# Kernel optimization log

Measured on AMD Instinct MI355X. Metric: run time of the kernel, lower is better.

## Reference

```python
import jax, jax.numpy as jnp
import numpy as np

H = 256
EDGE_DIM = 16
B, N = 8, 4096
E = 524288
EPS = 1e-5


def setup_inputs() -> dict:
    key = jax.random.key(0)
    ks = jax.random.split(key, 16)
    s = 0.02
    return {
        "h": jax.random.normal(ks[0], (B, N, H), dtype=jnp.float32),
        "edge_index": jax.random.randint(ks[1], (2, E), 0, B * N, dtype=jnp.int64),
        "edge_attr": jax.random.normal(ks[2], (E, EDGE_DIM), dtype=jnp.float32),
        "mask": jnp.ones((B, N), dtype=jnp.float32),
        # message_net params
        "W1": jax.random.normal(ks[3], (2 * H + EDGE_DIM, H), dtype=jnp.float32) * s,
        "b1": jnp.zeros((H,), dtype=jnp.float32),
        "W2": jax.random.normal(ks[4], (H, H), dtype=jnp.float32) * s,
        "b2": jnp.zeros((H,), dtype=jnp.float32),
        # update_net params
        "U1": jax.random.normal(ks[5], (2 * H, H), dtype=jnp.float32) * s,
        "c1": jnp.zeros((H,), dtype=jnp.float32),
        "U2": jax.random.normal(ks[6], (H, H), dtype=jnp.float32) * s,
        "c2": jnp.zeros((H,), dtype=jnp.float32),
        # LayerNorm params
        "gamma": jnp.ones((H,), dtype=jnp.float32),
        "beta": jnp.zeros((H,), dtype=jnp.float32),
    }


def reference(h, edge_index, edge_attr, mask, W1, b1, W2, b2, U1, c1, U2, c2, gamma, beta):
    batch, n_nodes, hid = h.shape
    h_flat = h.reshape(-1, hid)                       # (B*N, H)
    src, dst = edge_index[0], edge_index[1]
    # gather -> message MLP
    msg_in = jnp.concatenate([h_flat[src], h_flat[dst], edge_attr], axis=-1)  # (E, 2H+16)
    messages = jax.nn.silu(msg_in @ W1 + b1) @ W2 + b2                        # (E, H)
    # scatter-add aggregation by destination node
    aggr = jax.ops.segment_sum(messages, dst, num_segments=batch * n_nodes)   # (B*N, H)
    # update MLP + residual (dropout = identity in eval mode)
    upd_in = jnp.concatenate([h_flat, aggr], axis=-1)                         # (B*N, 2H)
    h_new = h_flat + (jax.nn.silu(upd_in @ U1 + c1) @ U2 + c2)
    # LayerNorm over last dim
    mu = jnp.mean(h_new, axis=-1, keepdims=True)
    var = jnp.mean(jnp.square(h_new - mu), axis=-1, keepdims=True)
    h_new = (h_new - mu) * jax.lax.rsqrt(var + EPS) * gamma + beta
    return h_new.reshape(batch, n_nodes, hid) * mask[..., None]
```

## Files before the change

kernel.cpp:

```cpp
#include <hip/hip_runtime.h>

#define H_DIM 256
#define E_NUM 524288
#define NN    32768
#define K2    512
#define K2S   520
#define SAS   264
#define XS    264

typedef unsigned short u16;
typedef unsigned int   u32;
typedef __attribute__((ext_vector_type(8))) short s16x8;
typedef __attribute__((ext_vector_type(4))) float f32x4;
typedef __attribute__((ext_vector_type(4))) unsigned short u16x4;

__device__ __forceinline__ u16 f2b(float x) {
    u32 u = __float_as_uint(x);
    u32 r = (u + 0x7FFFu + ((u >> 16) & 1u)) >> 16;
    return (u16)r;
}
__device__ __forceinline__ float b2f(u16 v) {
    u32 u = ((u32)v) << 16;
    return __uint_as_float(u);
}
__device__ __forceinline__ void fma4(float4& acc, float s, const float4& vw) {
    acc.x += s * vw.x; acc.y += s * vw.y; acc.z += s * vw.z; acc.w += s * vw.w;
}

__global__ __launch_bounds__(256) void k_prep_w(
    const float* __restrict__ W1, const float* __restrict__ W2,
    const float* __restrict__ U1, const float* __restrict__ U2,
    u16* __restrict__ WpqT, u16* __restrict__ W2T,
    u16* __restrict__ U1T, u16* __restrict__ U2T) {
    int idx = blockIdx.x * 256 + threadIdx.x;
    if (idx < 131072) {
        int c = idx >> 8, k = idx & 255;
        float v = (c < 256) ? W1[k * 256 + c] : W1[(256 + k) * 256 + (c - 256)];
        WpqT[idx] = f2b(v);
    } else if (idx < 196608) {
        int i = idx - 131072; int c = i >> 8, k = i & 255;
        W2T[i] = f2b(W2[k * 256 + c]);
    } else if (idx < 327680) {
        int i = idx - 196608; int c = i >> 9, k = i & 511;
        U1T[i] = f2b(U1[(size_t)k * 256 + c]);
    } else if (idx < 393216) {
        int i = idx - 327680; int c = i >> 8, k = i & 255;
        U2T[i] = f2b(U2[k * 256 + c]);
    }
}

__global__ __launch_bounds__(256) void k_hist(const int* __restrict__ eidx,
                                              int* __restrict__ cnt) {
    int i = blockIdx.x * 256 + threadIdx.x;
    if (i < E_NUM) atomicAdd(&cnt[eidx[E_NUM + i]], 1);
}

__global__ __launch_bounds__(256) void k_scan(const int* __restrict__ cnt,
                                              int* __restrict__ base,
                                              int* __restrict__ nxt) {
    __shared__ int part[256];
    const int t = threadIdx.x;
    const int st = t * 128;
    int s = 0;
    for (int i = 0; i < 128; ++i) s += cnt[st + i];
    part[t] = s;
    __syncthreads();
    if (t == 0) {
        int r = 0;
        for (int i = 0; i < 256; ++i) { int v = part[i]; part[i] = r; r += v; }
        base[NN] = r;
    }
    __syncthreads();
    int off = part[t];
    for (int i = 0; i < 128; ++i) {
        int v = cnt[st + i];
        base[st + i] = off;
        nxt[st + i] = off;
        off += v;
    }
}

__global__ __launch_bounds__(256) void k_scatter(const int* __restrict__ eidx,
                                                 int* __restrict__ nxt,
                                                 int2* __restrict__ elist) {
    int i = blockIdx.x * 256 + threadIdx.x;
    if (i < E_NUM) {
        int d = eidx[E_NUM + i];
        int p = atomicAdd(&nxt[d], 1);
        elist[p] = make_int2(eidx[i], i);
    }
}

__global__ __launch_bounds__(256, 2) void k_gemm_pq(
    const float* __restrict__ h, const u16* __restrict__ WpqT,
    u16* __restrict__ PQ) {
    __shared__ __align__(16) u16 sA[64 * SAS];
    const int t = threadIdx.x;
    const int rowTile = blockIdx.x >> 1, q = blockIdx.x & 1;
    const int n0 = rowTile * 64;
    {
        const int r = t >> 2, g = t & 3;
        const float* hrow = h + (size_t)(n0 + r) * 256;
        u16* rowp = sA + r * SAS;
#pragma unroll
        for (int j = 0; j < 8; ++j) {
            const int c = g + 4 * j;
            float4 v0 = *reinterpret_cast<const float4*>(hrow + c * 8);
            float4 v1 = *reinterpret_cast<const float4*>(hrow + c * 8 + 4);
            s16x8 o;
            o[0] = (short)f2b(v0.x); o[1] = (short)f2b(v0.y);
            o[2] = (short)f2b(v0.z); o[3] = (short)f2b(v0.w);
            o[4] = (short)f2b(v1.x); o[5] = (short)f2b(v1.y);
            o[6] = (short)f2b(v1.z); o[7] = (short)f2b(v1.w);
            *reinterpret_cast<s16x8*>(rowp + c * 8) = o;
        }
    }
    __syncthreads();
    const int lane = t & 63, wv = t >> 6;
    const int l15 = lane & 15, l4 = lane >> 4;
    const int colBase = wv * 64 + l15;
    const f32x4 z4 = {0.f, 0.f, 0.f, 0.f};
    f32x4 acc[4][4];
#pragma unroll
    for (int m = 0; m < 4; ++m)
#pragma unroll
        for (int n = 0; n < 4; ++n) acc[m][n] = z4;
    {
        const u16* Bb = WpqT + (size_t)(q * 256 + colBase) * 256 + l4 * 8;
        for (int kk = 0; kk < 8; ++kk) {
            s16x8 a[4], b[4];
#pragma unroll
            for (int m = 0; m < 4; ++m)
                a[m] = *reinterpret_cast<const s16x8*>(sA + (m * 16 + l15) * SAS + kk * 32 + l4 * 8);
#pragma unroll
            for (int n = 0; n < 4; ++n)
                b[n] = *reinterpret_cast<const s16x8*>(Bb + (size_t)n * 16 * 256 + kk * 32);
#pragma unroll
            for (int m = 0; m < 4; ++m)
#pragma unroll
                for (int n = 0; n < 4; ++n)
                    acc[m][n] = __builtin_amdgcn_mfma_f32_16x16x32_bf16(a[m], b[n], acc[m][n], 0, 0, 0);
        }
    }
#pragma unroll
    for (int m = 0; m < 4; ++m)
#pragma unroll
        for (int j = 0; j < 4; ++j) {
            const int row = n0 + m * 16 + l4 * 4 + j;
            u16* op = PQ + (size_t)row * 512 + q * 256 + colBase;
#pragma unroll
            for (int n = 0; n < 4; ++n) op[n * 16] = f2b(acc[m][n][j]);
        }
}

__global__ __launch_bounds__(256, 4) void k_aggr(
    const u16* __restrict__ PQ, const int2* __restrict__ elist,
    const int* __restrict__ base, const float* __restrict__ ea,
    const float* __restrict__ W1, const float* __restrict__ b1,
    u16* __restrict__ Sb) {
    const int t = threadIdx.x, lane = t & 63, wv = t >> 6;
    const int d = blockIdx.x * 4 + wv;
    const int c0 = lane * 4;
    float4 Wr[16];
#pragma unroll
    for (int k = 0; k < 16; ++k)
        Wr[k] = *reinterpret_cast<const float4*>(W1 + (size_t)(512 + k) * 256 + c0);
    float4 qb = *reinterpret_cast<const float4*>(b1 + c0);
    {
        u16x4 qv = *reinterpret_cast<const u16x4*>(PQ + (size_t)d * 512 + 256 + c0);
        qb.x += b2f(qv.x); qb.y += b2f(qv.y); qb.z += b2f(qv.z); qb.w += b2f(qv.w);
    }
    const int e0 = base[d], e1 = base[d + 1];
    float4 acc = {0.f, 0.f, 0.f, 0.f};
    for (int cb = e0; cb < e1; cb += 64) {
        const int n = min(64, e1 - cb);
        int2 ee = make_int2(0, 0);
        if (lane < n) ee = elist[cb + lane];
        int src = __shfl(ee.x, 0), eid = __shfl(ee.y, 0);
        u16x4 pv = *reinterpret_cast<const u16x4*>(PQ + (size_t)src * 512 + c0);
        const float* ep = ea + (size_t)eid * 16;
        float4 a0 = *reinterpret_cast<const float4*>(ep);
        float4 a1 = *reinterpret_cast<const float4*>(ep + 4);
        float4 a2 = *reinterpret_cast<const float4*>(ep + 8);
        float4 a3 = *reinterpret_cast<const float4*>(ep + 12);
        for (int k = 0; k < n; ++k) {
            const u16x4 pc = pv;
            const float4 e0v = a0, e1v = a1, e2v = a2, e3v = a3;
            if (k + 1 < n) {
                src = __shfl(ee.x, k + 1); eid = __shfl(ee.y, k + 1);
                pv = *reinterpret_cast<const u16x4*>(PQ + (size_t)src * 512 + c0);
                const float* ep2 = ea + (size_t)eid * 16;
                a0 = *reinterpret_cast<const float4*>(ep2);
                a1 = *reinterpret_cast<const float4*>(ep2 + 4);
                a2 = *reinterpret_cast<const float4*>(ep2 + 8);
                a3 = *reinterpret_cast<const float4*>(ep2 + 12);
            }
            float4 x = qb;
            x.x += b2f(pc.x); x.y += b2f(pc.y); x.z += b2f(pc.z); x.w += b2f(pc.w);
            fma4(x, e0v.x, Wr[0]);  fma4(x, e0v.y, Wr[1]);
            fma4(x, e0v.z, Wr[2]);  fma4(x, e0v.w, Wr[3]);
            fma4(x, e1v.x, Wr[4]);  fma4(x, e1v.y, Wr[5]);
            fma4(x, e1v.z, Wr[6]);  fma4(x, e1v.w, Wr[7]);
            fma4(x, e2v.x, Wr[8]);  fma4(x, e2v.y, Wr[9]);
            fma4(x, e2v.z, Wr[10]); fma4(x, e2v.w, Wr[11]);
            fma4(x, e3v.x, Wr[12]); fma4(x, e3v.y, Wr[13]);
            fma4(x, e3v.z, Wr[14]); fma4(x, e3v.w, Wr[15]);
            acc.x += x.x / (1.f + __expf(-x.x));
            acc.y += x.y / (1.f + __expf(-x.y));
            acc.z += x.z / (1.f + __expf(-x.z));
            acc.w += x.w / (1.f + __expf(-x.w));
        }
    }
    u16x4 o;
    o.x = f2b(acc.x); o.y = f2b(acc.y); o.z = f2b(acc.z); o.w = f2b(acc.w);
    *reinterpret_cast<u16x4*>(Sb + (size_t)d * 256 + c0) = o;
}

__global__ __launch_bounds__(256, 2) void k_gemm_s(
    const u16* __restrict__ Sb, const u16* __restrict__ W2T,
    const int* __restrict__ base, const float* __restrict__ b2,
    u16* __restrict__ aggrb) {
    __shared__ __align__(16) u16 sA[64 * SAS];
    const int t = threadIdx.x;
    const int n0 = blockIdx.x * 64;
    {
        const int r = t >> 2, g = t & 3;
        const u16* srow = Sb + (size_t)(n0 + r) * 256;
        u16* rowp = sA + r * SAS;
#pragma unroll
        for (int j = 0; j < 8; ++j) {
            const int c = g + 4 * j;
            *reinterpret_cast<s16x8*>(rowp + c * 8) =
                *reinterpret_cast<const s16x8*>(srow + c * 8);
        }
    }
    __syncthreads();
    const int lane = t & 63, wv = t >> 6;
    const int l15 = lane & 15, l4 = lane >> 4;
    const int colBase = wv * 64 + l15;
    const f32x4 z4 = {0.f, 0.f, 0.f, 0.f};
    f32x4 acc[4][4];
#pragma unroll
    for (int m = 0; m < 4; ++m)
#pragma unroll
        for (int n = 0; n < 4; ++n) acc[m][n] = z4;
    {
        const u16* Bb = W2T + (size_t)colBase * 256 + l4 * 8;
        for (int kk = 0; kk < 8; ++kk) {
            s16x8 a[4], b[4];
#pragma unroll
            for (int m = 0; m < 4; ++m)
                a[m] = *reinterpret_cast<const s16x8*>(sA + (m * 16 + l15) * SAS + kk * 32 + l4 * 8);
#pragma unroll
            for (int n = 0; n < 4; ++n)
                b[n] = *reinterpret_cast<const s16x8*>(Bb + (size_t)n * 16 * 256 + kk * 32);
#pragma unroll
            for (int m = 0; m < 4; ++m)
#pragma unroll
                for (int n = 0; n < 4; ++n)
                    acc[m][n] = __builtin_amdgcn_mfma_f32_16x16x32_bf16(a[m], b[n], acc[m][n], 0, 0, 0);
        }
    }
    float b2v[4];
#pragma unroll
    for (int n = 0; n < 4; ++n) b2v[n] = b2[colBase + n * 16];
#pragma unroll
    for (int m = 0; m < 4; ++m)
#pragma unroll
        for (int j = 0; j < 4; ++j) {
            const int row = n0 + m * 16 + l4 * 4 + j;
            const float dv = (float)(base[row + 1] - base[row]);
            u16* op = aggrb + (size_t)row * 256 + colBase;
#pragma unroll
            for (int n = 0; n < 4; ++n) op[n * 16] = f2b(acc[m][n][j] + dv * b2v[n]);
        }
}

__global__ __launch_bounds__(256, 2) void k_nodes(
    const float* __restrict__ h, const u16* __restrict__ aggrb,
    const u16* __restrict__ U1T, const u16* __restrict__ U2T,
    const float* __restrict__ c1, const float* __restrict__ c2,
    const float* __restrict__ gamma, const float* __restrict__ beta,
    const float* __restrict__ mask,
    float* __restrict__ out) {
    __shared__ __align__(16) char smemraw[64 * XS * 4];
    u16* sA = reinterpret_cast<u16*>(smemraw);
    const int t  = threadIdx.x;
    const int n0 = blockIdx.x * 64;

    {
        const int r = t >> 2, g = t & 3;
        const int node = n0 + r;
        const float* hrow = h + (size_t)node * H_DIM;
        const u16* arow = aggrb + (size_t)node * H_DIM;
        u16* rowp = sA + r * K2S;
#pragma unroll
        for (int j = 0; j < 16; ++j) {
            const int c = g + 4 * j;
            if (c < 32) {
                float4 v0 = *reinterpret_cast<const float4*>(hrow + c * 8);
                float4 v1 = *reinterpret_cast<const float4*>(hrow + c * 8 + 4);
                s16x8 o;
                o[0] = (short)f2b(v0.x); o[1] = (short)f2b(v0.y);
                o[2] = (short)f2b(v0.z); o[3] = (short)f2b(v0.w);
                o[4] = (short)f2b(v1.x); o[5] = (short)f2b(v1.y);
                o[6] = (short)f2b(v1.z); o[7] = (short)f2b(v1.w);
                *reinterpret_cast<s16x8*>(rowp + c * 8) = o;
            } else {
                const int cc = c - 32;
                *reinterpret_cast<s16x8*>(rowp + 256 + cc * 8) =
                    *reinterpret_cast<const s16x8*>(arow + cc * 8);
            }
        }
    }
    __syncthreads();

    const int lane = t & 63, wv = t >> 6;
    const int l15 = lane & 15, l4 = lane >> 4;
    const int colBase = wv * 64 + l15;
    const f32x4 z4 = {0.f, 0.f, 0.f, 0.f};

    f32x4 acc[4][4];
#pragma unroll
    for (int m = 0; m < 4; ++m)
#pragma unroll
        for (int n = 0; n < 4; ++n) acc[m][n] = z4;

    {
        const u16* Bb = U1T + (size_t)colBase * K2 + l4 * 8;
        for (int kk = 0; kk < 16; ++kk) {
            s16x8 a[4], b[4];
#pragma unroll
            for (int m = 0; m < 4; ++m)
                a[m] = *reinterpret_cast<const s16x8*>(sA + (m * 16 + l15) * K2S + kk * 32 + l4 * 8);
#pragma unroll
            for (int n = 0; n < 4; ++n)
                b[n] = *reinterpret_cast<const s16x8*>(Bb + (size_t)n * 16 * K2 + kk * 32);
#pragma unroll
            for (int m = 0; m < 4; ++m)
#pragma unroll
                for (int n = 0; n < 4; ++n)
                    acc[m][n] = __builtin_amdgcn_mfma_f32_16x16x32_bf16(a[m], b[n], acc[m][n], 0, 0, 0);
        }
    }
    __syncthreads();

    {
        u16* sX = reinterpret_cast<u16*>(smemraw);
        float c1v[4];
#pragma unroll
        for (int n = 0; n < 4; ++n) c1v[n] = c1[colBase + n * 16];
#pragma unroll
        for (int m = 0; m < 4; ++m)
#pragma unroll
            for (int n = 0; n < 4; ++n)
#pragma unroll
                for (int j = 0; j < 4; ++j) {
                    float x = acc[m][n][j] + c1v[n];
                    float s = x / (1.f + __expf(-x));
                    sX[(m * 16 + l4 * 4 + j) * XS + colBase + n * 16] = f2b(s);
                }
    }
    __syncthreads();

#pragma unroll
    for (int m = 0; m < 4; ++m)
#pragma unroll
        for (int n = 0; n < 4; ++n) acc[m][n] = z4;
    {
        const u16* sX = reinterpret_cast<u16*>(smemraw);
        const u16* Bb = U2T + (size_t)colBase * H_DIM + l4 * 8;
        for (int kk = 0; kk < 8; ++kk) {
            s16x8 a[4], b[4];
#pragma unroll
            for (int m = 0; m < 4; ++m)
                a[m] = *reinterpret_cast<const s16x8*>(sX + (m * 16 + l15) * XS + kk * 32 + l4 * 8);
#pragma unroll
            for (int n = 0; n < 4; ++n)
                b[n] = *reinterpret_cast<const s16x8*>(Bb + (size_t)n * 16 * H_DIM + kk * 32);
#pragma unroll
            for (int m = 0; m < 4; ++m)
#pragma unroll
                for (int n = 0; n < 4; ++n)
                    acc[m][n] = __builtin_amdgcn_mfma_f32_16x16x32_bf16(a[m], b[n], acc[m][n], 0, 0, 0);
        }
    }
    __syncthreads();

    {
        float* sF = reinterpret_cast<float*>(smemraw);
        float c2v[4];
#pragma unroll
        for (int n = 0; n < 4; ++n) c2v[n] = c2[colBase + n * 16];
#pragma unroll
        for (int m = 0; m < 4; ++m)
#pragma unroll
            for (int n = 0; n < 4; ++n)
#pragma unroll
                for (int j = 0; j < 4; ++j) {
                    const int row = m * 16 + l4 * 4 + j;
                    const float hv = h[(size_t)(n0 + row) * H_DIM + colBase + n * 16];
                    sF[row * XS + colBase + n * 16] = acc[m][n][j] + c2v[n] + hv;
                }
    }
    __syncthreads();

    {
        const float* sF = reinterpret_cast<const float*>(smemraw);
        const int rr = t >> 2, p = t & 3;
        const float* rowf = sF + rr * XS + p * 64;
        float s1 = 0.f, s2 = 0.f;
#pragma unroll
        for (int i = 0; i < 64; ++i) { float v = rowf[i]; s1 += v; s2 += v * v; }
        s1 += __shfl_xor(s1, 1); s1 += __shfl_xor(s1, 2);
        s2 += __shfl_xor(s2, 1); s2 += __shfl_xor(s2, 2);
        const float mu   = s1 * (1.f / 256.f);
        const float var  = s2 * (1.f / 256.f) - mu * mu;
        const float rstd = rsqrtf(var + 1e-5f);
        const int node = n0 + rr;
        const float mk = mask[node];
        float* op = out + (size_t)node * H_DIM + p * 64;
        const float* gp = gamma + p * 64;
        const float* bp = beta + p * 64;
#pragma unroll
        for (int i = 0; i < 64; i += 4) {
            float4 x  = *reinterpret_cast<const float4*>(rowf + i);
            float4 g4 = *reinterpret_cast<const float4*>(gp + i);
            float4 b4 = *reinterpret_cast<const float4*>(bp + i);
            float4 o;
            o.x = (((x.x - mu) * rstd) * g4.x + b4.x) * mk;
            o.y = (((x.y - mu) * rstd) * g4.y + b4.y) * mk;
            o.z = (((x.z - mu) * rstd) * g4.z + b4.z) * mk;
            o.w = (((x.w - mu) * rstd) * g4.w + b4.w) * mk;
            *reinterpret_cast<float4*>(op + i) = o;
        }
    }
}

#define OFF_PQ     0ull
#define OFF_SB     33554432ull
#define OFF_AGGRB  50331648ull
#define OFF_WPQT   67108864ull
#define OFF_W2T    67371008ull
#define OFF_U1T    67502080ull
#define OFF_U2T    67764224ull
#define OFF_CNT    67895296ull
#define OFF_BASE   68026368ull
#define OFF_NEXT   68157696ull
#define OFF_ELIST  68288768ull

extern "C" void kernel_launch(void* const* d_in, const int* in_sizes, int n_in,
                              void* d_out, int out_size, void* d_ws, size_t ws_size,
                              hipStream_t stream) {
    const float* h     = (const float*)d_in[0];
    const int*   eidx  = (const int*)d_in[1];
    const float* ea    = (const float*)d_in[2];
    const float* mask  = (const float*)d_in[3];
    const float* W1    = (const float*)d_in[4];
    const float* b1    = (const float*)d_in[5];
    const float* W2    = (const float*)d_in[6];
    const float* b2    = (const float*)d_in[7];
    const float* U1    = (const float*)d_in[8];
    const float* c1    = (const float*)d_in[9];
    const float* U2    = (const float*)d_in[10];
    const float* c2    = (const float*)d_in[11];
    const float* gamma = (const float*)d_in[12];
    const float* beta  = (const float*)d_in[13];
    float* out = (float*)d_out;
    char*  ws  = (char*)d_ws;

    u16*  PQ    = (u16*)(ws + OFF_PQ);
    u16*  Sb    = (u16*)(ws + OFF_SB);
    u16*  aggrb = (u16*)(ws + OFF_AGGRB);
    u16*  WpqT  = (u16*)(ws + OFF_WPQT);
    u16*  W2T   = (u16*)(ws + OFF_W2T);
    u16*  U1T   = (u16*)(ws + OFF_U1T);
    u16*  U2T   = (u16*)(ws + OFF_U2T);
    int*  cnt   = (int*)(ws + OFF_CNT);
    int*  base  = (int*)(ws + OFF_BASE);
    int*  nxt   = (int*)(ws + OFF_NEXT);
    int2* elist = (int2*)(ws + OFF_ELIST);

    hipMemsetAsync(cnt, 0, (size_t)NN * sizeof(int), stream);

    k_prep_w<<<1536, 256, 0, stream>>>(W1, W2, U1, U2, WpqT, W2T, U1T, U2T);
    k_hist<<<E_NUM / 256, 256, 0, stream>>>(eidx, cnt);
    k_scan<<<1, 256, 0, stream>>>(cnt, base, nxt);
    k_scatter<<<E_NUM / 256, 256, 0, stream>>>(eidx, nxt, elist);
    k_gemm_pq<<<(NN / 64) * 2, 256, 0, stream>>>(h, WpqT, PQ);
    k_aggr<<<NN / 4, 256, 0, stream>>>(PQ, elist, base, ea, W1, b1, Sb);
    k_gemm_s<<<NN / 64, 256, 0, stream>>>(Sb, W2T, base, b2, aggrb);
    k_nodes<<<NN / 64, 256, 0, stream>>>(h, aggrb, U1T, U2T, c1, c2, gamma, beta, mask, out);
}
```

Baseline: 339.5 us.

## Fuse W2 GEMM into node update kernel and vectorize aggregation with packed math

Merges the separate W2 GEMM kernel into the node update kernel: the S rows are staged in shared memory, multiplied by W2 (plus degree-scaled bias), and written back in place as the aggregate before the U1 GEMM. This removes one launch and the write and read of the intermediate aggregate buffer. The aggregation kernel now processes four nodes per wave, which amortizes the W1 edge-weight register loads. It also uses f32x2 vectors so the compiler can emit packed FMAs, and computes sigmoid with a fast reciprocal. The fused kernel adds extra syncs and does more work per block, and the rcp approximation slightly changes numerics.

```diff
diff --git a/kernel.cpp b/kernel.cpp
--- a/kernel.cpp
+++ b/kernel.cpp
@@ -7,11 +7,13 @@
 #define K2S   520
 #define SAS   264
 #define XS    264
+#define NPW   4
 
 typedef unsigned short u16;
 typedef unsigned int   u32;
 typedef __attribute__((ext_vector_type(8))) short s16x8;
 typedef __attribute__((ext_vector_type(4))) float f32x4;
+typedef __attribute__((ext_vector_type(2))) float f32x2;
 typedef __attribute__((ext_vector_type(4))) unsigned short u16x4;
 
 __device__ __forceinline__ u16 f2b(float x) {
@@ -23,8 +25,8 @@
     u32 u = ((u32)v) << 16;
     return __uint_as_float(u);
 }
-__device__ __forceinline__ void fma4(float4& acc, float s, const float4& vw) {
-    acc.x += s * vw.x; acc.y += s * vw.y; acc.z += s * vw.z; acc.w += s * vw.w;
+__device__ __forceinline__ float fsig(float x) {
+    return __builtin_amdgcn_rcpf(1.f + __expf(-x));
 }
 
 __global__ __launch_bounds__(256) void k_prep_w(
@@ -159,125 +161,86 @@
     const float* __restrict__ W1, const float* __restrict__ b1,
     u16* __restrict__ Sb) {
     const int t = threadIdx.x, lane = t & 63, wv = t >> 6;
-    const int d = blockIdx.x * 4 + wv;
     const int c0 = lane * 4;
-    float4 Wr[16];
-#pragma unroll
-    for (int k = 0; k < 16; ++k)
-        Wr[k] = *reinterpret_cast<const float4*>(W1 + (size_t)(512 + k) * 256 + c0);
-    float4 qb = *reinterpret_cast<const float4*>(b1 + c0);
-    {
-        u16x4 qv = *reinterpret_cast<const u16x4*>(PQ + (size_t)d * 512 + 256 + c0);
-        qb.x += b2f(qv.x); qb.y += b2f(qv.y); qb.z += b2f(qv.z); qb.w += b2f(qv.w);
-    }
-    const int e0 = base[d], e1 = base[d + 1];
-    float4 acc = {0.f, 0.f, 0.f, 0.f};
-    for (int cb = e0; cb < e1; cb += 64) {
-        const int n = min(64, e1 - cb);
-        int2 ee = make_int2(0, 0);
-        if (lane < n) ee = elist[cb + lane];
-        int src = __shfl(ee.x, 0), eid = __shfl(ee.y, 0);
-        u16x4 pv = *reinterpret_cast<const u16x4*>(PQ + (size_t)src * 512 + c0);
-        const float* ep = ea + (size_t)eid * 16;
-        float4 a0 = *reinterpret_cast<const float4*>(ep);
-        float4 a1 = *reinterpret_cast<const float4*>(ep + 4);
-        float4 a2 = *reinterpret_cast<const float4*>(ep + 8);
-        float4 a3 = *reinterpret_cast<const float4*>(ep + 12);
-        for (int k = 0; k < n; ++k) {
-            const u16x4 pc = pv;
-            const float4 e0v = a0, e1v = a1, e2v = a2, e3v = a3;
-            if (k + 1 < n) {
-                src = __shfl(ee.x, k + 1); eid = __shfl(ee.y, k + 1);
-                pv = *reinterpret_cast<const u16x4*>(PQ + (size_t)src * 512 + c0);
-                const float* ep2 = ea + (size_t)eid * 16;
-                a0 = *reinterpret_cast<const float4*>(ep2);
-                a1 = *reinterpret_cast<const float4*>(ep2 + 4);
-                a2 = *reinterpret_cast<const float4*>(ep2 + 8);
-                a3 = *reinterpret_cast<const float4*>(ep2 + 12);
+    f32x2 WrL[16], WrH[16];
+#pragma unroll
+    for (int k = 0; k < 16; ++k) {
+        float4 w = *reinterpret_cast<const float4*>(W1 + (size_t)(512 + k) * 256 + c0);
+        WrL[k] = f32x2{w.x, w.y};
+        WrH[k] = f32x2{w.z, w.w};
+    }
+    const float4 b1v = *reinterpret_cast<const float4*>(b1 + c0);
+
+    const int dBase = (blockIdx.x * 4 + wv) * NPW;
+    for (int nn = 0; nn < NPW; ++nn) {
+        const int d = dBase + nn;
+        f32x2 qbL = {b1v.x, b1v.y}, qbH = {b1v.z, b1v.w};
+        {
+            u16x4 qv = *reinterpret_cast<const u16x4*>(PQ + (size_t)d * 512 + 256 + c0);
+            qbL[0] += b2f(qv.x); qbL[1] += b2f(qv.y);
+            qbH[0] += b2f(qv.z); qbH[1] += b2f(qv.w);
+        }
+        const int e0 = base[d], e1 = base[d + 1];
+        f32x2 accL = {0.f, 0.f}, accH = {0.f, 0.f};
+        for (int cb = e0; cb < e1; cb += 64) {
+            const int n = min(64, e1 - cb);
+            int2 ee = make_int2(0, 0);
+            if (lane < n) ee = elist[cb + lane];
+            int src = __shfl(ee.x, 0), eid = __shfl(ee.y, 0);
+            u16x4 pv = *reinterpret_cast<const u16x4*>(PQ + (size_t)src * 512 + c0);
+            const float* ep = ea + (size_t)eid * 16;
+            float4 a0 = *reinterpret_cast<const float4*>(ep);
+            float4 a1 = *reinterpret_cast<const float4*>(ep + 4);
+            float4 a2 = *reinterpret_cast<const float4*>(ep + 8);
+            float4 a3 = *reinterpret_cast<const float4*>(ep + 12);
+            for (int k = 0; k < n; ++k) {
+                const u16x4 pc = pv;
+                const float4 e0v = a0, e1v = a1, e2v = a2, e3v = a3;
+                if (k + 1 < n) {
+                    src = __shfl(ee.x, k + 1); eid = __shfl(ee.y, k + 1);
+                    pv = *reinterpret_cast<const u16x4*>(PQ + (size_t)src * 512 + c0);
+                    const float* ep2 = ea + (size_t)eid * 16;
+                    a0 = *reinterpret_cast<const float4*>(ep2);
+                    a1 = *reinterpret_cast<const float4*>(ep2 + 4);
+                    a2 = *reinterpret_cast<const float4*>(ep2 + 8);
+                    a3 = *reinterpret_cast<const float4*>(ep2 + 12);
+                }
+                f32x2 xL = qbL, xH = qbH;
+                xL[0] += b2f(pc.x); xL[1] += b2f(pc.y);
+                xH[0] += b2f(pc.z); xH[1] += b2f(pc.w);
+                xL = xL + WrL[0]  * e0v.x; xH = xH + WrH[0]  * e0v.x;
+                xL = xL + WrL[1]  * e0v.y; xH = xH + WrH[1]  * e0v.y;
+                xL = xL + WrL[2]  * e0v.z; xH = xH + WrH[2]  * e0v.z;
+                xL = xL + WrL[3]  * e0v.w; xH = xH + WrH[3]  * e0v.w;
+                xL = xL + WrL[4]  * e1v.x; xH = xH + WrH[4]  * e1v.x;
+                xL = xL + WrL[5]  * e1v.y; xH = xH + WrH[5]  * e1v.y;
+                xL = xL + WrL[6]  * e1v.z; xH = xH + WrH[6]  * e1v.z;
+                xL = xL + WrL[7]  * e1v.w; xH = xH + WrH[7]  * e1v.w;
+                xL = xL + WrL[8]  * e2v.x; xH = xH + WrH[8]  * e2v.x;
+                xL = xL + WrL[9]  * e2v.y; xH = xH + WrH[9]  * e2v.y;
+                xL = xL + WrL[10] * e2v.z; xH = xH + WrH[10] * e2v.z;
+                xL = xL + WrL[11] * e2v.w; xH = xH + WrH[11] * e2v.w;
+                xL = xL + WrL[12] * e3v.x; xH = xH + WrH[12] * e3v.x;
+                xL = xL + WrL[13] * e3v.y; xH = xH + WrH[13] * e3v.y;
+                xL = xL + WrL[14] * e3v.z; xH = xH + WrH[14] * e3v.z;
+                xL = xL + WrL[15] * e3v.w; xH = xH + WrH[15] * e3v.w;
+                accL[0] += xL[0] * fsig(xL[0]);
+                accL[1] += xL[1] * fsig(xL[1]);
+                accH[0] += xH[0] * fsig(xH[0]);
+                accH[1] += xH[1] * fsig(xH[1]);
             }
-            float4 x = qb;
-            x.x += b2f(pc.x); x.y += b2f(pc.y); x.z += b2f(pc.z); x.w += b2f(pc.w);
-            fma4(x, e0v.x, Wr[0]);  fma4(x, e0v.y, Wr[1]);
-            fma4(x, e0v.z, Wr[2]);  fma4(x, e0v.w, Wr[3]);
-            fma4(x, e1v.x, Wr[4]);  fma4(x, e1v.y, Wr[5]);
-            fma4(x, e1v.z, Wr[6]);  fma4(x, e1v.w, Wr[7]);
-            fma4(x, e2v.x, Wr[8]);  fma4(x, e2v.y, Wr[9]);
-            fma4(x, e2v.z, Wr[10]); fma4(x, e2v.w, Wr[11]);
-            fma4(x, e3v.x, Wr[12]); fma4(x, e3v.y, Wr[13]);
-            fma4(x, e3v.z, Wr[14]); fma4(x, e3v.w, Wr[15]);
-            acc.x += x.x / (1.f + __expf(-x.x));
-            acc.y += x.y / (1.f + __expf(-x.y));
-            acc.z += x.z / (1.f + __expf(-x.z));
-            acc.w += x.w / (1.f + __expf(-x.w));
-        }
-    }
-    u16x4 o;
-    o.x = f2b(acc.x); o.y = f2b(acc.y); o.z = f2b(acc.z); o.w = f2b(acc.w);
-    *reinterpret_cast<u16x4*>(Sb + (size_t)d * 256 + c0) = o;
-}
-
-__global__ __launch_bounds__(256, 2) void k_gemm_s(
-    const u16* __restrict__ Sb, const u16* __restrict__ W2T,
-    const int* __restrict__ base, const float* __restrict__ b2,
-    u16* __restrict__ aggrb) {
-    __shared__ __align__(16) u16 sA[64 * SAS];
-    const int t = threadIdx.x;
-    const int n0 = blockIdx.x * 64;
-    {
-        const int r = t >> 2, g = t & 3;
-        const u16* srow = Sb + (size_t)(n0 + r) * 256;
-        u16* rowp = sA + r * SAS;
-#pragma unroll
-        for (int j = 0; j < 8; ++j) {
-            const int c = g + 4 * j;
-            *reinterpret_cast<s16x8*>(rowp + c * 8) =
-                *reinterpret_cast<const s16x8*>(srow + c * 8);
-        }
-    }
-    __syncthreads();
-    const int lane = t & 63, wv = t >> 6;
-    const int l15 = lane & 15, l4 = lane >> 4;
-    const int colBase = wv * 64 + l15;
-    const f32x4 z4 = {0.f, 0.f, 0.f, 0.f};
-    f32x4 acc[4][4];
-#pragma unroll
-    for (int m = 0; m < 4; ++m)
-#pragma unroll
-        for (int n = 0; n < 4; ++n) acc[m][n] = z4;
-    {
-        const u16* Bb = W2T + (size_t)colBase * 256 + l4 * 8;
-        for (int kk = 0; kk < 8; ++kk) {
-            s16x8 a[4], b[4];
-#pragma unroll
-            for (int m = 0; m < 4; ++m)
-                a[m] = *reinterpret_cast<const s16x8*>(sA + (m * 16 + l15) * SAS + kk * 32 + l4 * 8);
-#pragma unroll
-            for (int n = 0; n < 4; ++n)
-                b[n] = *reinterpret_cast<const s16x8*>(Bb + (size_t)n * 16 * 256 + kk * 32);
-#pragma unroll
-            for (int m = 0; m < 4; ++m)
-#pragma unroll
-                for (int n = 0; n < 4; ++n)
-                    acc[m][n] = __builtin_amdgcn_mfma_f32_16x16x32_bf16(a[m], b[n], acc[m][n], 0, 0, 0);
-        }
-    }
-    float b2v[4];
-#pragma unroll
-    for (int n = 0; n < 4; ++n) b2v[n] = b2[colBase + n * 16];
-#pragma unroll
-    for (int m = 0; m < 4; ++m)
-#pragma unroll
-        for (int j = 0; j < 4; ++j) {
-            const int row = n0 + m * 16 + l4 * 4 + j;
-            const float dv = (float)(base[row + 1] - base[row]);
-            u16* op = aggrb + (size_t)row * 256 + colBase;
-#pragma unroll
-            for (int n = 0; n < 4; ++n) op[n * 16] = f2b(acc[m][n][j] + dv * b2v[n]);
-        }
-}
-
-__global__ __launch_bounds__(256, 2) void k_nodes(
-    const float* __restrict__ h, const u16* __restrict__ aggrb,
+        }
+        u16x4 o;
+        o.x = f2b(accL[0]); o.y = f2b(accL[1]);
+        o.z = f2b(accH[0]); o.w = f2b(accH[1]);
+        *reinterpret_cast<u16x4*>(Sb + (size_t)d * 256 + c0) = o;
+    }
+}
+
+__global__ __launch_bounds__(256, 2) void k_post(
+    const float* __restrict__ h, const u16* __restrict__ Sb,
+    const u16* __restrict__ W2T, const int* __restrict__ base,
+    const float* __restrict__ b2,
     const u16* __restrict__ U1T, const u16* __restrict__ U2T,
     const float* __restrict__ c1, const float* __restrict__ c2,
     const float* __restrict__ gamma, const float* __restrict__ beta,
@@ -292,7 +255,7 @@
         const int r = t >> 2, g = t & 3;
         const int node = n0 + r;
         const float* hrow = h + (size_t)node * H_DIM;
-        const u16* arow = aggrb + (size_t)node * H_DIM;
+        const u16* srow = Sb + (size_t)node * H_DIM;
         u16* rowp = sA + r * K2S;
 #pragma unroll
         for (int j = 0; j < 16; ++j) {
@@ -309,7 +272,7 @@
             } else {
                 const int cc = c - 32;
                 *reinterpret_cast<s16x8*>(rowp + 256 + cc * 8) =
-                    *reinterpret_cast<const s16x8*>(arow + cc * 8);
+                    *reinterpret_cast<const s16x8*>(srow + cc * 8);
             }
         }
     }
@@ -327,6 +290,46 @@
         for (int n = 0; n < 4; ++n) acc[m][n] = z4;
 
     {
+        const u16* Bb = W2T + (size_t)colBase * 256 + l4 * 8;
+        for (int kk = 0; kk < 8; ++kk) {
+            s16x8 a[4], b[4];
+#pragma unroll
+            for (int m = 0; m < 4; ++m)
+                a[m] = *reinterpret_cast<const s16x8*>(sA + (m * 16 + l15) * K2S + 256 + kk * 32 + l4 * 8);
+#pragma unroll
+            for (int n = 0; n < 4; ++n)
+                b[n] = *reinterpret_cast<const s16x8*>(Bb + (size_t)n * 16 * 256 + kk * 32);
+#pragma unroll
+            for (int m = 0; m < 4; ++m)
+#pragma unroll
+                for (int n = 0; n < 4; ++n)
+                    acc[m][n] = __builtin_amdgcn_mfma_f32_16x16x32_bf16(a[m], b[n], acc[m][n], 0, 0, 0);
+        }
+    }
+    __syncthreads();
+
+    {
+        float b2v[4];
+#pragma unroll
+        for (int n = 0; n < 4; ++n) b2v[n] = b2[colBase + n * 16];
+#pragma unroll
+        for (int m = 0; m < 4; ++m)
+#pragma unroll
+            for (int j = 0; j < 4; ++j) {
+                const int row = m * 16 + l4 * 4 + j;
+                const float dv = (float)(base[n0 + row + 1] - base[n0 + row]);
+#pragma unroll
+                for (int n = 0; n < 4; ++n)
+                    sA[row * K2S + 256 + colBase + n * 16] = f2b(acc[m][n][j] + dv * b2v[n]);
+            }
+    }
+    __syncthreads();
+
+#pragma unroll
+    for (int m = 0; m < 4; ++m)
+#pragma unroll
+        for (int n = 0; n < 4; ++n) acc[m][n] = z4;
+    {
         const u16* Bb = U1T + (size_t)colBase * K2 + l4 * 8;
         for (int kk = 0; kk < 16; ++kk) {
             s16x8 a[4], b[4];
@@ -357,7 +360,7 @@
 #pragma unroll
                 for (int j = 0; j < 4; ++j) {
                     float x = acc[m][n][j] + c1v[n];
-                    float s = x / (1.f + __expf(-x));
+                    float s = x * fsig(x);
                     sX[(m * 16 + l4 * 4 + j) * XS + colBase + n * 16] = f2b(s);
                 }
     }
@@ -439,15 +442,14 @@
 
 #define OFF_PQ     0ull
 #define OFF_SB     33554432ull
-#define OFF_AGGRB  50331648ull
-#define OFF_WPQT   67108864ull
-#define OFF_W2T    67371008ull
-#define OFF_U1T    67502080ull
-#define OFF_U2T    67764224ull
-#define OFF_CNT    67895296ull
-#define OFF_BASE   68026368ull
-#define OFF_NEXT   68157696ull
-#define OFF_ELIST  68288768ull
+#define OFF_WPQT   50331648ull
+#define OFF_W2T    50593792ull
+#define OFF_U1T    50724864ull
+#define OFF_U2T    50987008ull
+#define OFF_CNT    51118080ull
+#define OFF_BASE   51249152ull
+#define OFF_NEXT   51380480ull
+#define OFF_ELIST  51511552ull
 
 extern "C" void kernel_launch(void* const* d_in, const int* in_sizes, int n_in,
                               void* d_out, int out_size, void* d_ws, size_t ws_size,
@@ -471,7 +473,6 @@
 
     u16*  PQ    = (u16*)(ws + OFF_PQ);
     u16*  Sb    = (u16*)(ws + OFF_SB);
-    u16*  aggrb = (u16*)(ws + OFF_AGGRB);
     u16*  WpqT  = (u16*)(ws + OFF_WPQT);
     u16*  W2T   = (u16*)(ws + OFF_W2T);
     u16*  U1T   = (u16*)(ws + OFF_U1T);
@@ -488,7 +489,7 @@
     k_scan<<<1, 256, 0, stream>>>(cnt, base, nxt);
     k_scatter<<<E_NUM / 256, 256, 0, stream>>>(eidx, nxt, elist);
     k_gemm_pq<<<(NN / 64) * 2, 256, 0, stream>>>(h, WpqT, PQ);
-    k_aggr<<<NN / 4, 256, 0, stream>>>(PQ, elist, base, ea, W1, b1, Sb);
-    k_gemm_s<<<NN / 64, 256, 0, stream>>>(Sb, W2T, base, b2, aggrb);
-    k_nodes<<<NN / 64, 256, 0, stream>>>(h, aggrb, U1T, U2T, c1, c2, gamma, beta, mask, out);
-}
+    k_aggr<<<NN / (4 * NPW), 256, 0, stream>>>(PQ, elist, base, ea, W1, b1, Sb);
+    k_post<<<NN / 64, 256, 0, stream>>>(h, Sb, W2T, base, b2, U1T, U2T,
+                                        c1, c2, gamma, beta, mask, out);
+}
```

After: 326.5 us. -3.8%, faster.
